# Kernel tuning notes

Measured on AMD Instinct MI355X. Metric: run time of the kernel, lower is better.

Reference implementation:

```python
import jax, jax.numpy as jnp
import numpy as np

N_NODES = 20000
IN_CH = 512
HEADS = 8
CH = 64  # hidden_layer per head
E = 320000
E_LABEL = 100000


def setup_inputs() -> dict:
    key = jax.random.key(0)
    ks = jax.random.split(key, 8)
    x = jax.random.normal(ks[0], (N_NODES, IN_CH), dtype=jnp.float32)
    edge_index = jax.random.randint(ks[1], (2, E), 0, N_NODES)
    edge_label_index = jax.random.randint(ks[2], (2, E_LABEL), 0, N_NODES)
    # GATv2Conv params (share_weights=False, bias=True)
    sc = 1.0 / np.sqrt(IN_CH)
    W_l = jax.random.normal(ks[3], (IN_CH, HEADS * CH), dtype=jnp.float32) * sc
    W_r = jax.random.normal(ks[4], (IN_CH, HEADS * CH), dtype=jnp.float32) * sc
    att = jax.random.normal(ks[5], (HEADS, CH), dtype=jnp.float32) * (1.0 / np.sqrt(CH))
    bias = jnp.zeros((HEADS * CH,), dtype=jnp.float32)
    gamma = jnp.ones((HEADS * CH,), dtype=jnp.float32)
    beta = jnp.zeros((HEADS * CH,), dtype=jnp.float32)
    return {"x": x, "edge_index": edge_index, "edge_label_index": edge_label_index,
            "W_l": W_l, "W_r": W_r, "att": att, "bias": bias,
            "gamma": gamma, "beta": beta}


def reference(x, edge_index, edge_label_index, W_l, W_r, att, bias, gamma, beta):
    N = x.shape[0]
    H, C = att.shape
    src, dst = edge_index[0], edge_index[1]
    # GATv2Conv: separate source/target linear maps
    xl = (x @ W_l).reshape(N, H, C)
    xr = (x @ W_r).reshape(N, H, C)
    # per-edge attention logits (GATv2: leaky_relu BEFORE attention vector)
    e = jax.nn.leaky_relu(xl[src] + xr[dst], negative_slope=0.2)  # [E,H,C]
    alpha = jnp.einsum('ehc,hc->eh', e, att)                      # [E,H]
    # softmax over incoming edges of each destination node
    amax = jax.ops.segment_max(alpha, dst, num_segments=N)        # [N,H]
    alpha = jnp.exp(alpha - amax[dst])
    denom = jax.ops.segment_sum(alpha, dst, num_segments=N)       # [N,H]
    alpha = alpha / (denom[dst] + 1e-16)
    # scatter-add aggregation of attended source messages
    out = jax.ops.segment_sum(alpha[:, :, None] * xl[src], dst, num_segments=N)  # [N,H,C]
    out = out.reshape(N, H * C) + bias
    # BatchNorm1d (training-mode batch stats, eps=1e-5)
    mu = out.mean(axis=0)
    var = out.var(axis=0)
    out = (out - mu) * jax.lax.rsqrt(var + 1e-5) * gamma + beta
    out = jax.nn.relu(out)  # dropout is identity in deterministic reference
    # gather + dot-product link scoring
    s = out[edge_label_index[0]]
    t = out[edge_label_index[1]]
    return jnp.sum(s * t, axis=1)  # [E_LABEL]
```

## Files before the change

kernel.cpp:

```cpp
#include <hip/hip_runtime.h>
#include <hip/hip_bf16.h>
#include <cstdint>

#define IN_CH 512
#define HC    512
#define HEADS 8
#define NPACK 1024

typedef __attribute__((ext_vector_type(8))) short bf16x8;
typedef __attribute__((ext_vector_type(8))) ushort u16x8;
typedef __attribute__((ext_vector_type(4))) float f32x4;
typedef const __attribute__((address_space(1))) uint8_t* gaddr_t;
typedef __attribute__((address_space(3))) uint8_t* laddr_t;

__device__ inline ushort f2bf(float f) {
  uint32_t u = __float_as_uint(f);
  return (ushort)((u + 0x7fffu + ((u >> 16) & 1u)) >> 16);
}
__device__ inline float bf2f(ushort u) {
  return __uint_as_float(((uint32_t)u) << 16);
}

__global__ void cast_x(const float* __restrict__ x, ushort* __restrict__ xb, int n4) {
  const int i = blockIdx.x * blockDim.x + threadIdx.x;
  if (i >= n4) return;
  const float4 v = ((const float4*)x)[i];
  ushort4 o;
  o.x = f2bf(v.x); o.y = f2bf(v.y); o.z = f2bf(v.z); o.w = f2bf(v.w);
  ((ushort4*)xb)[i] = o;
}

__global__ void pack_w(const float* __restrict__ Wl, const float* __restrict__ Wr,
                       ushort* __restrict__ bt) {
  const int i = blockIdx.x * blockDim.x + threadIdx.x;
  if (i >= NPACK * IN_CH) return;
  const int n = i >> 9, k = i & 511;
  const float v = (n < HC) ? Wl[(size_t)k * HC + n] : Wr[(size_t)k * HC + (n - HC)];
  bt[i] = f2bf(v);
}

__global__ __launch_bounds__(256) void gemm_mfma(
    const ushort* __restrict__ xb, const ushort* __restrict__ bt,
    ushort* __restrict__ xlb, float* __restrict__ xr, int M) {
  __shared__ __align__(16) ushort As[128 * 32];
  __shared__ __align__(16) ushort Bs[128 * 32];
  const int wave = threadIdx.x >> 6, lane = threadIdx.x & 63;
  const int row0 = blockIdx.y * 128, col0 = blockIdx.x * 128;
  const int quad = lane >> 4, m16 = lane & 15;
  const int wrow = (wave >> 1) * 64, wcol = (wave & 1) * 64;
  const int srow = lane >> 2;
  const int scol = (lane & 3) * 8;
  const f32x4 zero = {0.f, 0.f, 0.f, 0.f};
  f32x4 acc[4][4];
  #pragma unroll
  for (int i = 0; i < 4; ++i)
    #pragma unroll
    for (int j = 0; j < 4; ++j) acc[i][j] = zero;

  for (int k0 = 0; k0 < IN_CH; k0 += 32) {
    #pragma unroll
    for (int c = 0; c < 2; ++c) {
      const int chunk = wave * 2 + c;
      const ushort* ga = xb + (size_t)(row0 + chunk * 16 + srow) * IN_CH + k0 + scol;
      __builtin_amdgcn_global_load_lds((gaddr_t)ga, (laddr_t)(As + chunk * 512), 16, 0, 0);
      const ushort* gb = bt + (size_t)(col0 + chunk * 16 + srow) * IN_CH + k0 + scol;
      __builtin_amdgcn_global_load_lds((gaddr_t)gb, (laddr_t)(Bs + chunk * 512), 16, 0, 0);
    }
    __syncthreads();
    bf16x8 af[4], bfr[4];
    #pragma unroll
    for (int i = 0; i < 4; ++i)
      af[i] = *(const bf16x8*)(As + (wrow + i * 16 + m16) * 32 + quad * 8);
    #pragma unroll
    for (int j = 0; j < 4; ++j)
      bfr[j] = *(const bf16x8*)(Bs + (wcol + j * 16 + m16) * 32 + quad * 8);
    #pragma unroll
    for (int i = 0; i < 4; ++i)
      #pragma unroll
      for (int j = 0; j < 4; ++j)
        acc[i][j] = __builtin_amdgcn_mfma_f32_16x16x32_bf16(af[i], bfr[j], acc[i][j], 0, 0, 0);
    __syncthreads();
  }
  const bool isL = (col0 < HC);
  #pragma unroll
  for (int i = 0; i < 4; ++i) {
    const int r = row0 + wrow + i * 16 + quad * 4;
    #pragma unroll
    for (int j = 0; j < 4; ++j) {
      const int cg = col0 + wcol + j * 16 + m16;
      #pragma unroll
      for (int t = 0; t < 4; ++t) {
        const int rr = r + t;
        if (rr < M) {
          if (isL) xlb[(size_t)rr * HC + cg] = f2bf(acc[i][j][t]);
          else     xr[(size_t)rr * HC + (cg - HC)] = acc[i][j][t];
        }
      }
    }
  }
}

__global__ void hist_dst(const int* __restrict__ ei, int* __restrict__ counts, int E) {
  const int e = blockIdx.x * blockDim.x + threadIdx.x;
  if (e < E) atomicAdd(&counts[ei[E + e]], 1);
}

__global__ void scan1(const int* __restrict__ counts, int* __restrict__ offsets,
                      int* __restrict__ bsums, int Nn) {
  __shared__ int tmp[256];
  const int t = threadIdx.x;
  const int i = blockIdx.x * 256 + t;
  const int v = (i < Nn) ? counts[i] : 0;
  tmp[t] = v;
  __syncthreads();
  for (int d = 1; d < 256; d <<= 1) {
    int add = (t >= d) ? tmp[t - d] : 0;
    __syncthreads();
    tmp[t] += add;
    __syncthreads();
  }
  if (i < Nn) offsets[i] = tmp[t] - v;
  if (t == 255) bsums[blockIdx.x] = tmp[255];
}

__global__ void scan2(int* __restrict__ bsums, int nb) {
  __shared__ int tmp[256];
  const int t = threadIdx.x;
  if (t < nb) tmp[t] = bsums[t];
  __syncthreads();
  if (t == 0) {
    int run = 0;
    for (int b = 0; b < nb; ++b) { int c = tmp[b]; tmp[b] = run; run += c; }
  }
  __syncthreads();
  if (t < nb) bsums[t] = tmp[t];
}

__global__ void scan3(int* __restrict__ offsets, const int* __restrict__ bsums,
                      int* __restrict__ cursor, int Nn) {
  const int i = blockIdx.x * blockDim.x + threadIdx.x;
  if (i < Nn) {
    const int o = offsets[i] + bsums[i >> 8];
    offsets[i] = o;
    cursor[i] = o;
  }
}

__global__ void csr_fill(const int* __restrict__ ei, int* __restrict__ cursor,
                         int* __restrict__ csr_src, int E) {
  const int e = blockIdx.x * blockDim.x + threadIdx.x;
  if (e < E) {
    const int pos = atomicAdd(&cursor[ei[E + e]], 1);
    csr_src[pos] = ei[e];
  }
}

__global__ __launch_bounds__(256) void gatv2_agg(
    const ushort* __restrict__ xlb, const float* xr, const float* __restrict__ att,
    const int* __restrict__ offsets, const int* __restrict__ counts,
    const int* __restrict__ csr_src, float* agg, int Nn) {
  const int node = blockIdx.x * 4 + (threadIdx.x >> 6);
  const int lane = threadIdx.x & 63;
  if (node >= Nn) return;
  const int start = offsets[node];
  const int deg   = counts[node];
  const float4* pr = (const float4*)(xr + (size_t)node * HC + lane * 8);
  const float4 r0 = pr[0], r1 = pr[1];
  const float4* pa = (const float4*)(att + lane * 8);
  const float4 t0 = pa[0], t1 = pa[1];
  float acc[8] = {};
  float densum = 0.f;
  auto lrelu = [](float v) { return v > 0.f ? v : 0.2f * v; };

  u16x8 vb = {};
  if (deg > 0) {
    const int s0 = csr_src[start];
    vb = *(const u16x8*)(xlb + (size_t)s0 * HC + lane * 8);
  }
  for (int i = 0; i < deg; ++i) {
    const u16x8 cur = vb;
    if (i + 1 < deg) {
      const int sn = csr_src[start + i + 1];
      vb = *(const u16x8*)(xlb + (size_t)sn * HC + lane * 8);
    }
    float a[8];
    #pragma unroll
    for (int c = 0; c < 8; ++c) a[c] = bf2f((ushort)cur[c]);
    float s = lrelu(a[0] + r0.x) * t0.x + lrelu(a[1] + r0.y) * t0.y +
              lrelu(a[2] + r0.z) * t0.z + lrelu(a[3] + r0.w) * t0.w +
              lrelu(a[4] + r1.x) * t1.x + lrelu(a[5] + r1.y) * t1.y +
              lrelu(a[6] + r1.z) * t1.z + lrelu(a[7] + r1.w) * t1.w;
    s += __shfl_xor(s, 1, 8);
    s += __shfl_xor(s, 2, 8);
    s += __shfl_xor(s, 4, 8);
    const float ea = __expf(s);
    densum += ea;
    #pragma unroll
    for (int c = 0; c < 8; ++c) acc[c] += ea * a[c];
  }
  const float inv = 1.0f / (densum + 1e-16f);
  float* pd = agg + (size_t)node * HC + lane * 8;
  *(float4*)(pd + 0) = make_float4(acc[0] * inv, acc[1] * inv, acc[2] * inv, acc[3] * inv);
  *(float4*)(pd + 4) = make_float4(acc[4] * inv, acc[5] * inv, acc[6] * inv, acc[7] * inv);
}

__global__ void bn_stats(const float* __restrict__ agg, float* __restrict__ gsum,
                         float* __restrict__ gsq, int Nn) {
  const int t = threadIdx.x;
  const int rows_per_block = (Nn + gridDim.x - 1) / gridDim.x;
  const int r0 = blockIdx.x * rows_per_block;
  const int r1 = min(Nn, r0 + rows_per_block);
  float s0 = 0.f, s1 = 0.f, q0 = 0.f, q1 = 0.f;
  for (int r = r0; r < r1; ++r) {
    const float v0 = agg[(size_t)r * HC + t];
    const float v1 = agg[(size_t)r * HC + t + 256];
    s0 += v0; q0 += v0 * v0;
    s1 += v1; q1 += v1 * v1;
  }
  atomicAdd(&gsum[t], s0);
  atomicAdd(&gsum[t + 256], s1);
  atomicAdd(&gsq[t], q0);
  atomicAdd(&gsq[t + 256], q1);
}

__global__ void bn_final(const float* __restrict__ gsum, const float* __restrict__ gsq,
                         float* __restrict__ mu, float* __restrict__ rs, float invN) {
  const int c = threadIdx.x;
  const float m = gsum[c] * invN;
  const float v = gsq[c] * invN - m * m;
  mu[c] = m;
  rs[c] = rsqrtf(v + 1e-5f);
}

__global__ void bn_apply(const float* __restrict__ agg, const float* __restrict__ mu,
                         const float* __restrict__ rs, const float* __restrict__ gamma,
                         const float* __restrict__ beta, ushort* __restrict__ y, int total4) {
  const int i = blockIdx.x * blockDim.x + threadIdx.x;
  if (i >= total4) return;
  const int base = i << 2;
  const int c = base & (HC - 1);
  float4 v = *(const float4*)(agg + base);
  ushort4 o;
  o.x = f2bf(fmaxf(0.f, (v.x - mu[c + 0]) * rs[c + 0] * gamma[c + 0] + beta[c + 0]));
  o.y = f2bf(fmaxf(0.f, (v.y - mu[c + 1]) * rs[c + 1] * gamma[c + 1] + beta[c + 1]));
  o.z = f2bf(fmaxf(0.f, (v.z - mu[c + 2]) * rs[c + 2] * gamma[c + 2] + beta[c + 2]));
  o.w = f2bf(fmaxf(0.f, (v.w - mu[c + 3]) * rs[c + 3] * gamma[c + 3] + beta[c + 3]));
  *(ushort4*)(y + base) = o;
}

__global__ void score(const ushort* __restrict__ y, const int* __restrict__ eli,
                      float* __restrict__ out, int EL) {
  const int wave = blockIdx.x * (blockDim.x >> 6) + (threadIdx.x >> 6);
  const int lane = threadIdx.x & 63;
  if (wave >= EL) return;
  const int a = eli[wave];
  const int b = eli[EL + wave];
  const u16x8 ua = *(const u16x8*)(y + (size_t)a * HC + lane * 8);
  const u16x8 ub = *(const u16x8*)(y + (size_t)b * HC + lane * 8);
  float s = 0.f;
  #pragma unroll
  for (int c = 0; c < 8; ++c) s += bf2f((ushort)ua[c]) * bf2f((ushort)ub[c]);
  #pragma unroll
  for (int off = 32; off > 0; off >>= 1) s += __shfl_down(s, off, 64);
  if (lane == 0) out[wave] = s;
}

extern "C" void kernel_launch(void* const* d_in, const int* in_sizes, int n_in,
                              void* d_out, int out_size, void* d_ws, size_t ws_size,
                              hipStream_t stream) {
  const float* x     = (const float*)d_in[0];
  const int*   ei    = (const int*)d_in[1];
  const int*   eli   = (const int*)d_in[2];
  const float* W_l   = (const float*)d_in[3];
  const float* W_r   = (const float*)d_in[4];
  const float* att   = (const float*)d_in[5];
  const float* gamma = (const float*)d_in[7];
  const float* beta  = (const float*)d_in[8];
  float* out = (float*)d_out;

  const int Nn = in_sizes[0] / IN_CH;
  const int E  = in_sizes[1] / 2;
  const int EL = in_sizes[2] / 2;

  ushort* xlb = (ushort*)d_ws;
  float*  xr  = (float*)(xlb + (size_t)Nn * HC);
  ushort* xbf = (ushort*)(xr + (size_t)Nn * HC);
  ushort* btb = xbf + (size_t)Nn * IN_CH;
  int* counts  = (int*)xbf;
  int* offsets = counts + Nn;
  int* cursor  = offsets + Nn;
  int* bsums   = cursor + Nn;
  int* csr_src = bsums + 256;
  float* gsum  = (float*)(csr_src + E);
  float* gsq   = gsum + HC;
  float* mu    = gsq + HC;
  float* rs    = mu + HC;
  float*  agg = xr;
  ushort* y   = xlb;

  const int nb = (Nn + 255) / 256;

  cast_x<<<(Nn * IN_CH / 4 + 255) / 256, 256, 0, stream>>>(x, xbf, Nn * IN_CH / 4);
  pack_w<<<(NPACK * IN_CH + 255) / 256, 256, 0, stream>>>(W_l, W_r, btb);
  dim3 ggrid(NPACK / 128, (Nn + 127) / 128);
  gemm_mfma<<<ggrid, 256, 0, stream>>>(xbf, btb, xlb, xr, Nn);

  hipMemsetAsync(counts, 0, Nn * sizeof(int), stream);
  hist_dst<<<(E + 255) / 256, 256, 0, stream>>>(ei, counts, E);
  scan1<<<nb, 256, 0, stream>>>(counts, offsets, bsums, Nn);
  scan2<<<1, 256, 0, stream>>>(bsums, nb);
  scan3<<<nb, 256, 0, stream>>>(offsets, bsums, cursor, Nn);
  csr_fill<<<(E + 255) / 256, 256, 0, stream>>>(ei, cursor, csr_src, E);

  gatv2_agg<<<(Nn + 3) / 4, 256, 0, stream>>>(xlb, xr, att, offsets, counts,
                                              csr_src, agg, Nn);

  hipMemsetAsync(gsum, 0, 2 * HC * sizeof(float), stream);
  bn_stats<<<200, 256, 0, stream>>>(agg, gsum, gsq, Nn);
  bn_final<<<1, HC, 0, stream>>>(gsum, gsq, mu, rs, 1.0f / (float)Nn);
  bn_apply<<<(Nn * HC / 4 + 255) / 256, 256, 0, stream>>>(agg, mu, rs, gamma, beta, y,
                                                          Nn * HC / 4);

  score<<<(EL + 3) / 4, 256, 0, stream>>>(y, eli, out, EL);
}
```

Baseline: 325.1 us.

## Fuse prep kernels, CSR-group link scoring by source, unroll aggregation loop

Merges the input cast, weight pack and destination histogram into one launch, and adds a second histogram and CSR build over edge_label_index sources, so scoring runs per source node and loads that node's row once for all its label edges. The GATv2 aggregation loop now keeps two rows in flight, and leaky-relu becomes an fmax form. Both scans are batched into shared launches and the memsets are merged. The trade-off is extra CSR construction work (atomics, writes of target and edge ids) to save repeated source-row gathers and a few launches.

```diff
diff --git a/kernel.cpp b/kernel.cpp
--- a/kernel.cpp
+++ b/kernel.cpp
@@ -21,22 +21,35 @@
   return __uint_as_float(((uint32_t)u) << 16);
 }
 
-__global__ void cast_x(const float* __restrict__ x, ushort* __restrict__ xb, int n4) {
-  const int i = blockIdx.x * blockDim.x + threadIdx.x;
-  if (i >= n4) return;
-  const float4 v = ((const float4*)x)[i];
-  ushort4 o;
-  o.x = f2bf(v.x); o.y = f2bf(v.y); o.z = f2bf(v.z); o.w = f2bf(v.w);
-  ((ushort4*)xb)[i] = o;
-}
-
-__global__ void pack_w(const float* __restrict__ Wl, const float* __restrict__ Wr,
-                       ushort* __restrict__ bt) {
-  const int i = blockIdx.x * blockDim.x + threadIdx.x;
-  if (i >= NPACK * IN_CH) return;
-  const int n = i >> 9, k = i & 511;
-  const float v = (n < HC) ? Wl[(size_t)k * HC + n] : Wr[(size_t)k * HC + (n - HC)];
-  bt[i] = f2bf(v);
+__global__ void prep(const float* __restrict__ x, ushort* __restrict__ xb,
+                     const float* __restrict__ Wl, const float* __restrict__ Wr,
+                     ushort* __restrict__ bt,
+                     const int* __restrict__ ei, int* __restrict__ counts,
+                     const int* __restrict__ eli, int* __restrict__ counts2,
+                     int n4, int E, int EL, int nbc, int nbp, int nbh) {
+  const int b = blockIdx.x;
+  if (b < nbc) {
+    const int i = b * 256 + threadIdx.x;
+    if (i < n4) {
+      const float4 v = ((const float4*)x)[i];
+      ushort4 o;
+      o.x = f2bf(v.x); o.y = f2bf(v.y); o.z = f2bf(v.z); o.w = f2bf(v.w);
+      ((ushort4*)xb)[i] = o;
+    }
+  } else if (b < nbc + nbp) {
+    const int i = (b - nbc) * 256 + threadIdx.x;
+    if (i < NPACK * IN_CH) {
+      const int n = i >> 9, k = i & 511;
+      const float v = (n < HC) ? Wl[(size_t)k * HC + n] : Wr[(size_t)k * HC + (n - HC)];
+      bt[i] = f2bf(v);
+    }
+  } else if (b < nbc + nbp + nbh) {
+    const int e = (b - nbc - nbp) * 256 + threadIdx.x;
+    if (e < E) atomicAdd(&counts[ei[E + e]], 1);
+  } else {
+    const int e = (b - nbc - nbp - nbh) * 256 + threadIdx.x;
+    if (e < EL) atomicAdd(&counts2[eli[e]], 1);
+  }
 }
 
 __global__ __launch_bounds__(256) void gemm_mfma(
@@ -100,16 +113,17 @@
   }
 }
 
-__global__ void hist_dst(const int* __restrict__ ei, int* __restrict__ counts, int E) {
-  const int e = blockIdx.x * blockDim.x + threadIdx.x;
-  if (e < E) atomicAdd(&counts[ei[E + e]], 1);
-}
-
-__global__ void scan1(const int* __restrict__ counts, int* __restrict__ offsets,
-                      int* __restrict__ bsums, int Nn) {
+__global__ void scan1(const int* __restrict__ cA, int* __restrict__ oA, int* __restrict__ bA,
+                      const int* __restrict__ cB, int* __restrict__ oB, int* __restrict__ bB,
+                      int Nn, int nb) {
+  const int half = (blockIdx.x >= nb) ? 1 : 0;
+  const int blk  = blockIdx.x - half * nb;
+  const int* counts = half ? cB : cA;
+  int* offsets = half ? oB : oA;
+  int* bsums   = half ? bB : bA;
   __shared__ int tmp[256];
   const int t = threadIdx.x;
-  const int i = blockIdx.x * 256 + t;
+  const int i = blk * 256 + t;
   const int v = (i < Nn) ? counts[i] : 0;
   tmp[t] = v;
   __syncthreads();
@@ -120,10 +134,11 @@
     __syncthreads();
   }
   if (i < Nn) offsets[i] = tmp[t] - v;
-  if (t == 255) bsums[blockIdx.x] = tmp[255];
-}
-
-__global__ void scan2(int* __restrict__ bsums, int nb) {
+  if (t == 255) bsums[blk] = tmp[255];
+}
+
+__global__ void scan2(int* __restrict__ bA, int* __restrict__ bB, int nb) {
+  int* bsums = blockIdx.x ? bB : bA;
   __shared__ int tmp[256];
   const int t = threadIdx.x;
   if (t < nb) tmp[t] = bsums[t];
@@ -136,9 +151,15 @@
   if (t < nb) bsums[t] = tmp[t];
 }
 
-__global__ void scan3(int* __restrict__ offsets, const int* __restrict__ bsums,
-                      int* __restrict__ cursor, int Nn) {
-  const int i = blockIdx.x * blockDim.x + threadIdx.x;
+__global__ void scan3(int* __restrict__ oA, const int* __restrict__ bA, int* __restrict__ curA,
+                      int* __restrict__ oB, const int* __restrict__ bB, int* __restrict__ curB,
+                      int Nn, int nb) {
+  const int half = (blockIdx.x >= nb) ? 1 : 0;
+  const int blk  = blockIdx.x - half * nb;
+  int* offsets = half ? oB : oA;
+  const int* bsums = half ? bB : bA;
+  int* cursor  = half ? curB : curA;
+  const int i = blk * 256 + threadIdx.x;
   if (i < Nn) {
     const int o = offsets[i] + bsums[i >> 8];
     offsets[i] = o;
@@ -147,11 +168,24 @@
 }
 
 __global__ void csr_fill(const int* __restrict__ ei, int* __restrict__ cursor,
-                         int* __restrict__ csr_src, int E) {
-  const int e = blockIdx.x * blockDim.x + threadIdx.x;
-  if (e < E) {
-    const int pos = atomicAdd(&cursor[ei[E + e]], 1);
-    csr_src[pos] = ei[e];
+                         int* __restrict__ csr_src,
+                         const int* __restrict__ eli, int* __restrict__ cursor2,
+                         int* __restrict__ csr_t, int* __restrict__ csr_eid,
+                         int E, int EL, int nbE) {
+  const int b = blockIdx.x;
+  if (b < nbE) {
+    const int e = b * 256 + threadIdx.x;
+    if (e < E) {
+      const int pos = atomicAdd(&cursor[ei[E + e]], 1);
+      csr_src[pos] = ei[e];
+    }
+  } else {
+    const int e = (b - nbE) * 256 + threadIdx.x;
+    if (e < EL) {
+      const int pos = atomicAdd(&cursor2[eli[e]], 1);
+      csr_t[pos] = eli[EL + e];
+      csr_eid[pos] = e;
+    }
   }
 }
 
@@ -164,32 +198,33 @@
   if (node >= Nn) return;
   const int start = offsets[node];
   const int deg   = counts[node];
-  const float4* pr = (const float4*)(xr + (size_t)node * HC + lane * 8);
-  const float4 r0 = pr[0], r1 = pr[1];
-  const float4* pa = (const float4*)(att + lane * 8);
-  const float4 t0 = pa[0], t1 = pa[1];
+  float rv[8], tv[8];
+  {
+    const float4* pr = (const float4*)(xr + (size_t)node * HC + lane * 8);
+    const float4 r0 = pr[0], r1 = pr[1];
+    rv[0]=r0.x; rv[1]=r0.y; rv[2]=r0.z; rv[3]=r0.w;
+    rv[4]=r1.x; rv[5]=r1.y; rv[6]=r1.z; rv[7]=r1.w;
+    const float4* pa = (const float4*)(att + lane * 8);
+    const float4 t0 = pa[0], t1 = pa[1];
+    tv[0]=t0.x; tv[1]=t0.y; tv[2]=t0.z; tv[3]=t0.w;
+    tv[4]=t1.x; tv[5]=t1.y; tv[6]=t1.z; tv[7]=t1.w;
+  }
   float acc[8] = {};
   float densum = 0.f;
-  auto lrelu = [](float v) { return v > 0.f ? v : 0.2f * v; };
-
-  u16x8 vb = {};
-  if (deg > 0) {
-    const int s0 = csr_src[start];
-    vb = *(const u16x8*)(xlb + (size_t)s0 * HC + lane * 8);
-  }
-  for (int i = 0; i < deg; ++i) {
-    const u16x8 cur = vb;
-    if (i + 1 < deg) {
-      const int sn = csr_src[start + i + 1];
-      vb = *(const u16x8*)(xlb + (size_t)sn * HC + lane * 8);
-    }
+  const int* ps = csr_src + start;
+  auto row = [&](int idx) {
+    return *(const u16x8*)(xlb + (size_t)ps[idx] * HC + lane * 8);
+  };
+  auto body = [&](const u16x8 cur) {
     float a[8];
     #pragma unroll
     for (int c = 0; c < 8; ++c) a[c] = bf2f((ushort)cur[c]);
-    float s = lrelu(a[0] + r0.x) * t0.x + lrelu(a[1] + r0.y) * t0.y +
-              lrelu(a[2] + r0.z) * t0.z + lrelu(a[3] + r0.w) * t0.w +
-              lrelu(a[4] + r1.x) * t1.x + lrelu(a[5] + r1.y) * t1.y +
-              lrelu(a[6] + r1.z) * t1.z + lrelu(a[7] + r1.w) * t1.w;
+    float s = 0.f;
+    #pragma unroll
+    for (int c = 0; c < 8; ++c) {
+      const float v = a[c] + rv[c];
+      s += fmaxf(v, 0.2f * v) * tv[c];
+    }
     s += __shfl_xor(s, 1, 8);
     s += __shfl_xor(s, 2, 8);
     s += __shfl_xor(s, 4, 8);
@@ -197,7 +232,22 @@
     densum += ea;
     #pragma unroll
     for (int c = 0; c < 8; ++c) acc[c] += ea * a[c];
-  }
+  };
+
+  u16x8 v0 = {}, v1 = {};
+  if (deg > 0) v0 = row(0);
+  if (deg > 1) v1 = row(1);
+  int i = 0;
+  for (; i + 2 <= deg; i += 2) {
+    const u16x8 c0 = v0;
+    if (i + 2 < deg) v0 = row(i + 2);
+    body(c0);
+    const u16x8 c1 = v1;
+    if (i + 3 < deg) v1 = row(i + 3);
+    body(c1);
+  }
+  if (i < deg) body(v0);
+
   const float inv = 1.0f / (densum + 1e-16f);
   float* pd = agg + (size_t)node * HC + lane * 8;
   *(float4*)(pd + 0) = make_float4(acc[0] * inv, acc[1] * inv, acc[2] * inv, acc[3] * inv);
@@ -248,21 +298,48 @@
   *(ushort4*)(y + base) = o;
 }
 
-__global__ void score(const ushort* __restrict__ y, const int* __restrict__ eli,
-                      float* __restrict__ out, int EL) {
-  const int wave = blockIdx.x * (blockDim.x >> 6) + (threadIdx.x >> 6);
+__global__ __launch_bounds__(256) void score_g(
+    const ushort* __restrict__ y, const int* __restrict__ off2,
+    const int* __restrict__ cnt2, const int* __restrict__ csr_t,
+    const int* __restrict__ csr_eid, float* __restrict__ out, int Nn) {
+  const int node = blockIdx.x * 4 + (threadIdx.x >> 6);
   const int lane = threadIdx.x & 63;
-  if (wave >= EL) return;
-  const int a = eli[wave];
-  const int b = eli[EL + wave];
-  const u16x8 ua = *(const u16x8*)(y + (size_t)a * HC + lane * 8);
-  const u16x8 ub = *(const u16x8*)(y + (size_t)b * HC + lane * 8);
-  float s = 0.f;
-  #pragma unroll
-  for (int c = 0; c < 8; ++c) s += bf2f((ushort)ua[c]) * bf2f((ushort)ub[c]);
-  #pragma unroll
-  for (int off = 32; off > 0; off >>= 1) s += __shfl_down(s, off, 64);
-  if (lane == 0) out[wave] = s;
+  if (node >= Nn) return;
+  const int start = off2[node];
+  const int deg   = cnt2[node];
+  if (deg == 0) return;
+  float a[8];
+  {
+    const u16x8 us = *(const u16x8*)(y + (size_t)node * HC + lane * 8);
+    #pragma unroll
+    for (int c = 0; c < 8; ++c) a[c] = bf2f((ushort)us[c]);
+  }
+  const int* pt = csr_t + start;
+  const int* pe = csr_eid + start;
+  auto row = [&](int idx) {
+    return *(const u16x8*)(y + (size_t)pt[idx] * HC + lane * 8);
+  };
+  auto emit = [&](const u16x8 ut, int eid) {
+    float s = 0.f;
+    #pragma unroll
+    for (int c = 0; c < 8; ++c) s += a[c] * bf2f((ushort)ut[c]);
+    #pragma unroll
+    for (int off = 32; off > 0; off >>= 1) s += __shfl_down(s, off, 64);
+    if (lane == 0) out[eid] = s;
+  };
+  u16x8 v0 = {}, v1 = {};
+  v0 = row(0);
+  if (deg > 1) v1 = row(1);
+  int j = 0;
+  for (; j + 2 <= deg; j += 2) {
+    const u16x8 c0 = v0;
+    if (j + 2 < deg) v0 = row(j + 2);
+    emit(c0, pe[j]);
+    const u16x8 c1 = v1;
+    if (j + 3 < deg) v1 = row(j + 3);
+    emit(c1, pe[j + 1]);
+  }
+  if (j < deg) emit(v0, pe[j]);
 }
 
 extern "C" void kernel_launch(void* const* d_in, const int* in_sizes, int n_in,
@@ -286,40 +363,55 @@
   float*  xr  = (float*)(xlb + (size_t)Nn * HC);
   ushort* xbf = (ushort*)(xr + (size_t)Nn * HC);
   ushort* btb = xbf + (size_t)Nn * IN_CH;
-  int* counts  = (int*)xbf;
-  int* offsets = counts + Nn;
-  int* cursor  = offsets + Nn;
-  int* bsums   = cursor + Nn;
-  int* csr_src = bsums + 256;
-  float* gsum  = (float*)(csr_src + E);
-  float* gsq   = gsum + HC;
-  float* mu    = gsq + HC;
-  float* rs    = mu + HC;
+  int* counts   = (int*)(btb + (size_t)NPACK * IN_CH);
+  int* counts2  = counts + Nn;
+  float* gsum   = (float*)(counts2 + Nn);
+  float* gsq    = gsum + HC;
+  int* offsets  = (int*)(gsq + HC);
+  int* cursor   = offsets + Nn;
+  int* bsumsA   = cursor + Nn;
+  int* offsets2 = bsumsA + 256;
+  int* cursor2  = offsets2 + Nn;
+  int* bsumsB   = cursor2 + Nn;
+  int* csr_src  = bsumsB + 256;
+  int* csr_t    = csr_src + E;
+  int* csr_eid  = csr_t + EL;
+  float* mu     = (float*)(csr_eid + EL);
+  float* rs     = mu + HC;
   float*  agg = xr;
   ushort* y   = xlb;
 
-  const int nb = (Nn + 255) / 256;
-
-  cast_x<<<(Nn * IN_CH / 4 + 255) / 256, 256, 0, stream>>>(x, xbf, Nn * IN_CH / 4);
-  pack_w<<<(NPACK * IN_CH + 255) / 256, 256, 0, stream>>>(W_l, W_r, btb);
+  const int nb  = (Nn + 255) / 256;
+  const int nbc = (Nn * IN_CH / 4 + 255) / 256;
+  const int nbp = (NPACK * IN_CH + 255) / 256;
+  const int nbh = (E + 255) / 256;
+  const int nbh2 = (EL + 255) / 256;
+
+  hipMemsetAsync(counts, 0, (2 * (size_t)Nn + 2 * HC) * sizeof(int), stream);
+
+  prep<<<nbc + nbp + nbh + nbh2, 256, 0, stream>>>(
+      x, xbf, W_l, W_r, btb, ei, counts, eli, counts2,
+      Nn * IN_CH / 4, E, EL, nbc, nbp, nbh);
+
   dim3 ggrid(NPACK / 128, (Nn + 127) / 128);
   gemm_mfma<<<ggrid, 256, 0, stream>>>(xbf, btb, xlb, xr, Nn);
 
-  hipMemsetAsync(counts, 0, Nn * sizeof(int), stream);
-  hist_dst<<<(E + 255) / 256, 256, 0, stream>>>(ei, counts, E);
-  scan1<<<nb, 256, 0, stream>>>(counts, offsets, bsums, Nn);
-  scan2<<<1, 256, 0, stream>>>(bsums, nb);
-  scan3<<<nb, 256, 0, stream>>>(offsets, bsums, cursor, Nn);
-  csr_fill<<<(E + 255) / 256, 256, 0, stream>>>(ei, cursor, csr_src, E);
+  scan1<<<2 * nb, 256, 0, stream>>>(counts, offsets, bsumsA,
+                                    counts2, offsets2, bsumsB, Nn, nb);
+  scan2<<<2, 256, 0, stream>>>(bsumsA, bsumsB, nb);
+  scan3<<<2 * nb, 256, 0, stream>>>(offsets, bsumsA, cursor,
+                                    offsets2, bsumsB, cursor2, Nn, nb);
+  csr_fill<<<nbh + nbh2, 256, 0, stream>>>(ei, cursor, csr_src,
+                                           eli, cursor2, csr_t, csr_eid, E, EL, nbh);
 
   gatv2_agg<<<(Nn + 3) / 4, 256, 0, stream>>>(xlb, xr, att, offsets, counts,
                                               csr_src, agg, Nn);
 
-  hipMemsetAsync(gsum, 0, 2 * HC * sizeof(float), stream);
   bn_stats<<<200, 256, 0, stream>>>(agg, gsum, gsq, Nn);
   bn_final<<<1, HC, 0, stream>>>(gsum, gsq, mu, rs, 1.0f / (float)Nn);
   bn_apply<<<(Nn * HC / 4 + 255) / 256, 256, 0, stream>>>(agg, mu, rs, gamma, beta, y,
                                                           Nn * HC / 4);
 
-  score<<<(EL + 3) / 4, 256, 0, stream>>>(y, eli, out, EL);
-}
+  score_g<<<(Nn + 3) / 4, 256, 0, stream>>>(y, offsets2, counts2, csr_t, csr_eid,
+                                            out, Nn);
+}
```

After: 320.1 us. Within noise of the previous version (-1.5%).
